# Kernel optimization log

Measured on AMD Instinct MI355X. Metric: run time of the kernel, lower is better.

The kernel has to match this reference:

```python
import jax, jax.numpy as jnp
import numpy as np

LN_EPS = 1e-12  # BERT LayerNorm eps


def _lstm_dir(x, wih, whh, bih, bhh, reverse):
    # x: [T, B, D] -> outputs [T, B, Hd]; torch gate order i, f, g, o
    B = x.shape[1]
    Hd = whh.shape[1]
    b = bih + bhh

    def step(carry, xt):
        h, c = carry
        gates = xt @ wih.T + h @ whh.T + b  # [B, 4*Hd]
        i, f, g, o = jnp.split(gates, 4, axis=-1)
        c = jax.nn.sigmoid(f) * c + jax.nn.sigmoid(i) * jnp.tanh(g)
        h = jax.nn.sigmoid(o) * jnp.tanh(c)
        return (h, c), h

    init = (jnp.zeros((B, Hd), x.dtype), jnp.zeros((B, Hd), x.dtype))
    _, ys = jax.lax.scan(step, init, x, reverse=reverse)
    return ys


def _forward(input_ids, labels, word_emb, pos_emb, type_emb, ln_g, ln_b,
             w_ih, w_hh, b_ih, b_hh, fc_w, fc_b, crf_start, crf_end, crf_trans):
    B, T = input_ids.shape
    # BERT embeddings (eval mode: dropout = identity)
    emb = word_emb[input_ids] + pos_emb[:T][None, :, :] + type_emb[0][None, None, :]
    mu = emb.mean(-1, keepdims=True)
    var = ((emb - mu) ** 2).mean(-1, keepdims=True)
    emb = (emb - mu) / jnp.sqrt(var + LN_EPS) * ln_g + ln_b

    # stacked bidirectional LSTM
    x = emb.transpose(1, 0, 2)  # [T, B, 768]
    n_layers = w_ih.shape[0]
    for l in range(n_layers):
        f = _lstm_dir(x, w_ih[l, 0], w_hh[l, 0], b_ih[l, 0], b_hh[l, 0], False)
        r = _lstm_dir(x, w_ih[l, 1], w_hh[l, 1], b_ih[l, 1], b_hh[l, 1], True)
        x = jnp.concatenate([f, r], axis=-1)  # [T, B, 768]
    out = x.transpose(1, 0, 2)  # [B, T, 768]

    em = out @ fc_w.T + fc_b  # emissions [B, T, C]

    # CRF log-likelihood (full mask, torchcrf reduction='sum')
    gold_em = jnp.take_along_axis(em, labels[..., None], axis=2)[..., 0]  # [B, T]
    score = (crf_start[labels[:, 0]]
             + gold_em.sum(axis=1)
             + crf_trans[labels[:, :-1], labels[:, 1:]].sum(axis=1)
             + crf_end[labels[:, -1]])

    alpha0 = crf_start[None, :] + em[:, 0]  # [B, C]

    def step(alpha, e_t):
        a = jax.nn.logsumexp(alpha[:, :, None] + crf_trans[None, :, :], axis=1) + e_t
        return a, None

    alpha, _ = jax.lax.scan(step, alpha0, em[:, 1:].transpose(1, 0, 2))
    logZ = jax.nn.logsumexp(alpha + crf_end[None, :], axis=1)  # [B]
    return jnp.sum(logZ - score)  # loss = -llh


def setup_inputs() -> dict:
    key = jax.random.key(0)
    ks = jax.random.split(key, 16)
    B, T, V, P, D, C, L, Hd = 32, 256, 30522, 512, 768, 14, 2, 384
    s = 0.05
    return {
        "input_ids": jax.random.randint(ks[0], (B, T), 0, V),
        "labels": jax.random.randint(ks[1], (B, T), 0, C),
        "word_emb": jax.random.normal(ks[2], (V, D), jnp.float32) * 0.02,
        "pos_emb": jax.random.normal(ks[3], (P, D), jnp.float32) * 0.02,
        "type_emb": jax.random.normal(ks[4], (2, D), jnp.float32) * 0.02,
        "ln_g": jnp.ones((D,), jnp.float32),
        "ln_b": jnp.zeros((D,), jnp.float32),
        "w_ih": jax.random.normal(ks[5], (L, 2, 4 * Hd, D), jnp.float32) * s,
        "w_hh": jax.random.normal(ks[6], (L, 2, 4 * Hd, Hd), jnp.float32) * s,
        "b_ih": jax.random.normal(ks[7], (L, 2, 4 * Hd), jnp.float32) * s,
        "b_hh": jax.random.normal(ks[8], (L, 2, 4 * Hd), jnp.float32) * s,
        "fc_w": jax.random.normal(ks[9], (C, D), jnp.float32) * s,
        "fc_b": jnp.zeros((C,), jnp.float32),
        "crf_start": jax.random.normal(ks[10], (C,), jnp.float32) * 0.1,
        "crf_end": jax.random.normal(ks[11], (C,), jnp.float32) * 0.1,
        "crf_trans": jax.random.normal(ks[12], (C, C), jnp.float32) * 0.1,
    }


def reference(input_ids, labels, word_emb, pos_emb, type_emb, ln_g, ln_b,
              w_ih, w_hh, b_ih, b_hh, fc_w, fc_b, crf_start, crf_end, crf_trans):
    return _forward(input_ids, labels, word_emb, pos_emb, type_emb, ln_g, ln_b,
                    w_ih, w_hh, b_ih, b_hh, fc_w, fc_b, crf_start, crf_end, crf_trans)
```

## Files before the change

kernel.cpp:

```cpp
#include <hip/hip_runtime.h>

typedef unsigned short u16;
typedef unsigned long long u64;
typedef __bf16 bfx8 __attribute__((ext_vector_type(8)));
typedef float  fx4  __attribute__((ext_vector_type(4)));

static __device__ __forceinline__ float b2f(u16 u){
  unsigned v = ((unsigned)u) << 16;
  return __builtin_bit_cast(float, v);
}
static __device__ __forceinline__ u16 f2b(float f){
  unsigned u = __builtin_bit_cast(unsigned, f);
  u = (u + 0x7FFFu + ((u >> 16) & 1u)) >> 16;
  return (u16)u;
}
static __device__ __forceinline__ float blo(unsigned v){ return b2f((u16)(v & 0xFFFFu)); }
static __device__ __forceinline__ float bhi(unsigned v){ return b2f((u16)(v >> 16)); }
static __device__ __forceinline__ float sigm(float x){
  float cx = fminf(fmaxf(x, -30.f), 30.f);
  float e = __expf(-cx);
  return __builtin_amdgcn_rcpf(1.f + e);
}
static __device__ __forceinline__ float tanh_f(float x){
  float cx = fminf(fmaxf(x, -15.f), 15.f);
  float e = __expf(2.f * cx);
  return (e - 1.f) * __builtin_amdgcn_rcpf(e + 1.f);
}
static __device__ __forceinline__ u64 ald64(const u64* p){
  return __hip_atomic_load(p, __ATOMIC_RELAXED, __HIP_MEMORY_SCOPE_AGENT);
}
static __device__ __forceinline__ void ast64(u64* p, u64 v){
  __hip_atomic_store(p, v, __ATOMIC_RELAXED, __HIP_MEMORY_SCOPE_AGENT);
}

__global__ __launch_bounds__(256) void embed_ln(
    const int* __restrict__ ids, const float* __restrict__ we,
    const float* __restrict__ pe, const float* __restrict__ te,
    const float* __restrict__ lng, const float* __restrict__ lnb,
    u16* __restrict__ X)
{
  int row = blockIdx.x;
  int t = row >> 5, b = row & 31;
  int id = ids[b * 256 + t];
  int tid = threadIdx.x;
  int wv = tid >> 6, lane = tid & 63;
  __shared__ float red[8];
  float v[3]; float s = 0.f, s2 = 0.f;
  const float* wrow = we + (long)id * 768;
  const float* prow = pe + (long)t * 768;
#pragma unroll
  for (int u = 0; u < 3; ++u){
    int k = tid + 256 * u;
    float x = wrow[k] + prow[k] + te[k];
    v[u] = x; s += x; s2 += x * x;
  }
#pragma unroll
  for (int o = 32; o > 0; o >>= 1){ s += __shfl_xor(s, o); s2 += __shfl_xor(s2, o); }
  if (lane == 0){ red[wv] = s; red[4 + wv] = s2; }
  __syncthreads();
  float S  = red[0] + red[1] + red[2] + red[3];
  float S2 = red[4] + red[5] + red[6] + red[7];
  float mu = S * (1.f / 768.f);
  float var = S2 * (1.f / 768.f) - mu * mu;
  float rs = rsqrtf(var + 1e-12f);
#pragma unroll
  for (int u = 0; u < 3; ++u){
    int k = tid + 256 * u;
    float y = (v[u] - mu) * rs * lng[k] + lnb[k];
    X[(long)row * 768 + k] = f2b(y);
  }
}

__global__ __launch_bounds__(256) void gemm_pre(
    const u16* __restrict__ A,
    const float* __restrict__ W,
    const float* __restrict__ bi,
    const float* __restrict__ bh,
    u16* __restrict__ pre)
{
  __shared__ u16 la[64][40];
  __shared__ u16 lb[64][40];
  int m0 = blockIdx.x * 64, n0 = blockIdx.y * 64;
  int tid = threadIdx.x;
  int wv = tid >> 6, lane = tid & 63;
  int l15 = lane & 15, l4 = lane >> 4;
  int r = tid >> 2, seg = (tid & 3) * 8;
  fx4 acc[4];
#pragma unroll
  for (int i = 0; i < 4; ++i){ acc[i][0]=0.f; acc[i][1]=0.f; acc[i][2]=0.f; acc[i][3]=0.f; }
  for (int k0 = 0; k0 < 768; k0 += 32){
    __syncthreads();
    *reinterpret_cast<uint4*>(&la[r][seg]) =
        *reinterpret_cast<const uint4*>(&A[(long)(m0 + r) * 768 + k0 + seg]);
    {
      const float* src = &W[(long)(n0 + r) * 768 + k0 + seg];
      union { u16 h[8]; uint4 v; } tb;
#pragma unroll
      for (int e = 0; e < 8; ++e) tb.h[e] = f2b(src[e]);
      *reinterpret_cast<uint4*>(&lb[r][seg]) = tb.v;
    }
    __syncthreads();
    bfx8 af = __builtin_bit_cast(bfx8, *reinterpret_cast<const uint4*>(&la[wv * 16 + l15][8 * l4]));
#pragma unroll
    for (int nt = 0; nt < 4; ++nt){
      bfx8 bf = __builtin_bit_cast(bfx8, *reinterpret_cast<const uint4*>(&lb[nt * 16 + l15][8 * l4]));
      acc[nt] = __builtin_amdgcn_mfma_f32_16x16x32_bf16(af, bf, acc[nt], 0, 0, 0);
    }
  }
#pragma unroll
  for (int nt = 0; nt < 4; ++nt){
    int n = n0 + nt * 16 + l15;
    int d = (n >= 1536) ? 1 : 0;
    int np = n - d * 1536;
    float bias = bi[n] + bh[n];
#pragma unroll
    for (int q = 0; q < 4; ++q){
      int m = m0 + wv * 16 + 4 * l4 + q;
      int tt = m >> 5, bb = m & 31;
      float vv = acc[nt][q] + bias;
      pre[((long)((d * 256 + tt) * 32 + bb)) * 1536 + np] = f2b(vv);
    }
  }
}

__global__ __launch_bounds__(256) void lstm_layer(
    const float* __restrict__ Whh,
    const u16*  __restrict__ pre,
    u16* __restrict__ Y,
    u64* __restrict__ H64)
{
  __shared__ u16 lw[64][386];
  __shared__ u16 hb[32][386];
  __shared__ float gl2[4][16][33];
  int wg = blockIdx.x;
  int d = wg / 24, sl = wg - d * 24;
  int js = sl * 16;
  int tid = threadIdx.x;
  int wv = tid >> 6, lane = tid & 63;
  int l15 = lane & 15, l4 = lane >> 4;
  int b0 = tid & 31, q = tid >> 5;
  int jl0 = 2 * q, jl1 = 2 * q + 1;

  ast64(&H64[((long)(1 * 2 + d) * 192 + sl * 8 + q) * 32 + b0], 0ull);

  for (int i = tid; i < 64 * 96; i += 256){
    int rr = i / 96, c4 = i - rr * 96;
    const float* src = Whh + ((long)(d * 1536 + (rr >> 4) * 384 + js + (rr & 15))) * 384 + 4 * c4;
    float4 v = *reinterpret_cast<const float4*>(src);
    short4 pk;
    pk.x = (short)f2b(v.x); pk.y = (short)f2b(v.y);
    pk.z = (short)f2b(v.z); pk.w = (short)f2b(v.w);
    *reinterpret_cast<short4*>(&lw[rr][(4 * c4) ^ (8 * (rr & 7))]) = pk;
  }
  __syncthreads();

  float c0 = 0.f, c1 = 0.f;

  int tfirst = d ? 255 : 0;
  const u16* pb0 = pre + ((long)(d * 256 + tfirst) * 32 + b0) * 1536 + js + jl0;
  uint4 pc;
  pc.x = *reinterpret_cast<const unsigned*>(pb0 + 0 * 384);
  pc.y = *reinterpret_cast<const unsigned*>(pb0 + 1 * 384);
  pc.z = *reinterpret_cast<const unsigned*>(pb0 + 2 * 384);
  pc.w = *reinterpret_cast<const unsigned*>(pb0 + 3 * 384);

  for (int s = 0; s < 256; ++s){
    int tt = d ? (255 - s) : s;
    int pr = (s + 1) & 1;
    int pw = s & 1;

    int sn = (s + 1 < 256) ? (s + 1) : 255;
    int tn = d ? (255 - sn) : sn;
    const u16* pb2 = pre + ((long)(d * 256 + tn) * 32 + b0) * 1536 + js + jl0;
    uint4 pn;
    pn.x = *reinterpret_cast<const unsigned*>(pb2 + 0 * 384);
    pn.y = *reinterpret_cast<const unsigned*>(pb2 + 1 * 384);
    pn.z = *reinterpret_cast<const unsigned*>(pb2 + 2 * 384);
    pn.w = *reinterpret_cast<const unsigned*>(pb2 + 3 * 384);

    {
      const u64* hsrc = H64 + (long)(pr * 2 + d) * 192 * 32;
      unsigned tagv = (unsigned)s;
      for (;;){
        u64 vb[24];
#pragma unroll
        for (int i = 0; i < 24; ++i) vb[i] = ald64(&hsrc[tid + 256 * i]);
        bool ok = true;
#pragma unroll
        for (int i = 0; i < 24; ++i) ok = ok && ((unsigned)(vb[i] >> 32) == tagv);
#pragma unroll
        for (int i = 0; i < 24; ++i){
          int f = tid + 256 * i;
          int bb = f & 31, j2 = f >> 5;
          *reinterpret_cast<unsigned*>(&hb[bb][(2 * j2) ^ (8 * (bb & 7))]) = (unsigned)vb[i];
        }
        if (__syncthreads_and((int)ok)) break;
      }
    }

    fx4 a0a, a0b, a1a, a1b;
#pragma unroll
    for (int z = 0; z < 4; ++z){ a0a[z]=0.f; a0b[z]=0.f; a1a[z]=0.f; a1b[z]=0.f; }
#pragma unroll
    for (int kk = 0; kk < 12; kk += 2){
      int col0 = (kk * 32 + 8 * l4) ^ (8 * (l15 & 7));
      int col1 = ((kk + 1) * 32 + 8 * l4) ^ (8 * (l15 & 7));
      bfx8 bw0 = __builtin_bit_cast(bfx8, *reinterpret_cast<const uint4*>(&lw[wv * 16 + l15][col0]));
      bfx8 h00 = __builtin_bit_cast(bfx8, *reinterpret_cast<const uint4*>(&hb[l15][col0]));
      bfx8 h10 = __builtin_bit_cast(bfx8, *reinterpret_cast<const uint4*>(&hb[16 + l15][col0]));
      bfx8 bw1 = __builtin_bit_cast(bfx8, *reinterpret_cast<const uint4*>(&lw[wv * 16 + l15][col1]));
      bfx8 h01 = __builtin_bit_cast(bfx8, *reinterpret_cast<const uint4*>(&hb[l15][col1]));
      bfx8 h11 = __builtin_bit_cast(bfx8, *reinterpret_cast<const uint4*>(&hb[16 + l15][col1]));
      a0a = __builtin_amdgcn_mfma_f32_16x16x32_bf16(h00, bw0, a0a, 0, 0, 0);
      a1a = __builtin_amdgcn_mfma_f32_16x16x32_bf16(h10, bw0, a1a, 0, 0, 0);
      a0b = __builtin_amdgcn_mfma_f32_16x16x32_bf16(h01, bw1, a0b, 0, 0, 0);
      a1b = __builtin_amdgcn_mfma_f32_16x16x32_bf16(h11, bw1, a1b, 0, 0, 0);
    }
#pragma unroll
    for (int qq = 0; qq < 4; ++qq){
      int bb0 = (4 * l4 + qq) ^ (4 * (l15 & 7));
      int bb1 = (16 + 4 * l4 + qq) ^ (4 * (l15 & 7));
      gl2[wv][l15][bb0] = a0a[qq] + a0b[qq];
      gl2[wv][l15][bb1] = a1a[qq] + a1b[qq];
    }
    __syncthreads();

    int x0 = b0 ^ (4 * (jl0 & 7));
    int x1 = b0 ^ (4 * (jl1 & 7));
    float gi0 = gl2[0][jl0][x0] + blo(pc.x), gi1 = gl2[0][jl1][x1] + bhi(pc.x);
    float gf0 = gl2[1][jl0][x0] + blo(pc.y), gf1 = gl2[1][jl1][x1] + bhi(pc.y);
    float gg0 = gl2[2][jl0][x0] + blo(pc.z), gg1 = gl2[2][jl1][x1] + bhi(pc.z);
    float go0 = gl2[3][jl0][x0] + blo(pc.w), go1 = gl2[3][jl1][x1] + bhi(pc.w);
    c0 = sigm(gf0) * c0 + sigm(gi0) * tanh_f(gg0);
    float h0 = sigm(go0) * tanh_f(c0);
    c1 = sigm(gf1) * c1 + sigm(gi1) * tanh_f(gg1);
    float h1 = sigm(go1) * tanh_f(c1);

    unsigned hv = (unsigned)f2b(h0) | ((unsigned)f2b(h1) << 16);
    ast64(&H64[((long)(pw * 2 + d) * 192 + sl * 8 + q) * 32 + b0],
          ((u64)(unsigned)(s + 1) << 32) | (u64)hv);
    *reinterpret_cast<unsigned*>(&Y[((long)tt * 32 + b0) * 768 + d * 384 + js + jl0]) = hv;
    pc = pn;
  }
}

__global__ __launch_bounds__(256) void fc_em(
    const u16* __restrict__ Y2, const float* __restrict__ fw,
    const float* __restrict__ fb, float* __restrict__ em)
{
  int row = blockIdx.x * 4 + (threadIdx.x >> 6);
  int lane = threadIdx.x & 63;
  float acc[14];
#pragma unroll
  for (int c = 0; c < 14; ++c) acc[c] = 0.f;
#pragma unroll
  for (int u = 0; u < 12; ++u){
    int k = lane + 64 * u;
    float y = b2f(Y2[(long)row * 768 + k]);
#pragma unroll
    for (int c = 0; c < 14; ++c) acc[c] += y * fw[c * 768 + k];
  }
#pragma unroll
  for (int c = 0; c < 14; ++c){
    float a = acc[c];
#pragma unroll
    for (int o = 32; o > 0; o >>= 1) a += __shfl_xor(a, o);
    acc[c] = a;
  }
  if (lane == 0){
    int tt = row >> 5, b = row & 31;
#pragma unroll
    for (int c = 0; c < 14; ++c) em[(long)(b * 256 + tt) * 14 + c] = acc[c] + fb[c];
  }
}

__global__ __launch_bounds__(64) void crf_fwd(
    const float* __restrict__ em,
    const int* __restrict__ labels,
    const float* __restrict__ cs, const float* __restrict__ ce,
    const float* __restrict__ ct,
    float* __restrict__ lossb)
{
  int b = blockIdx.x;
  int lane = threadIdx.x;
  const float* E = em + (long)b * 256 * 14;
  const int* L = labels + b * 256;

  float sc = 0.f;
  for (int t = lane; t < 256; t += 64){
    int lt = L[t];
    sc += E[t * 14 + lt];
    if (t < 255) sc += ct[lt * 14 + L[t + 1]];
  }
#pragma unroll
  for (int o = 32; o > 0; o >>= 1) sc += __shfl_xor(sc, o);
  float score = sc + cs[L[0]] + ce[L[255]];

  __shared__ float al[2][16];
  int j = lane >> 2, ih = lane & 3;
  if (lane < 16){
    al[0][lane] = (lane < 14) ? (cs[lane] + E[lane]) : -1e30f;
    al[1][lane] = -1e30f;
  }
  __syncthreads();
  float tr[4];
#pragma unroll
  for (int w = 0; w < 4; ++w){
    int i = ih * 4 + w;
    tr[w] = (i < 14 && j < 14) ? ct[i * 14 + j] : -1e30f;
  }
  for (int t = 1; t < 256; ++t){
    int par = t & 1;
    float vals[4]; float m = -1e30f;
#pragma unroll
    for (int w = 0; w < 4; ++w){
      int i = ih * 4 + w;
      float v = al[par ^ 1][i] + tr[w];
      vals[w] = v; m = fmaxf(m, v);
    }
    m = fmaxf(m, __shfl_xor(m, 1));
    m = fmaxf(m, __shfl_xor(m, 2));
    float s = 0.f;
#pragma unroll
    for (int w = 0; w < 4; ++w) s += __expf(vals[w] - m);
    s += __shfl_xor(s, 1);
    s += __shfl_xor(s, 2);
    if (ih == 0 && j < 14) al[par][j] = m + __logf(s) + E[t * 14 + j];
    __syncthreads();
  }
  float v = (lane < 14) ? (al[1][lane] + ce[lane]) : -1e30f;
  float mm = v;
#pragma unroll
  for (int o = 32; o > 0; o >>= 1) mm = fmaxf(mm, __shfl_xor(mm, o));
  float ss = (lane < 14) ? __expf(v - mm) : 0.f;
#pragma unroll
  for (int o = 32; o > 0; o >>= 1) ss += __shfl_xor(ss, o);
  if (lane == 0) lossb[b] = (mm + __logf(ss)) - score;
}

__global__ __launch_bounds__(64) void final_sum(const float* __restrict__ lb, float* __restrict__ out){
  int lane = threadIdx.x;
  float v = (lane < 32) ? lb[lane] : 0.f;
#pragma unroll
  for (int o = 32; o > 0; o >>= 1) v += __shfl_xor(v, o);
  if (lane == 0) out[0] = v;
}

extern "C" void kernel_launch(void* const* d_in, const int* in_sizes, int n_in,
                              void* d_out, int out_size, void* d_ws, size_t ws_size,
                              hipStream_t stream)
{
  const int*   ids = (const int*)d_in[0];
  const int*   lab = (const int*)d_in[1];
  const float* we  = (const float*)d_in[2];
  const float* pe  = (const float*)d_in[3];
  const float* te  = (const float*)d_in[4];
  const float* lng = (const float*)d_in[5];
  const float* lnb = (const float*)d_in[6];
  const float* wih = (const float*)d_in[7];
  const float* whh = (const float*)d_in[8];
  const float* bih = (const float*)d_in[9];
  const float* bhh = (const float*)d_in[10];
  const float* fcw = (const float*)d_in[11];
  const float* fcb = (const float*)d_in[12];
  const float* cs  = (const float*)d_in[13];
  const float* ce  = (const float*)d_in[14];
  const float* ct  = (const float*)d_in[15];
  float* out = (float*)d_out;

  char* ws = (char*)d_ws;
  size_t off = 0;
  u16* X0  = (u16*)(ws + off); off += (size_t)8192 * 768 * 2;
  u16* Y1  = (u16*)(ws + off); off += (size_t)8192 * 768 * 2;
  u16* PRE = (u16*)(ws + off); off += (size_t)2 * 256 * 32 * 1536 * 2;
  float* EM = (float*)(ws + off); off += (size_t)32 * 256 * 14 * 4;
  u64* H64a = (u64*)(ws + off); off += (size_t)2 * 2 * 192 * 32 * 8;
  u64* H64b = (u64*)(ws + off); off += (size_t)2 * 2 * 192 * 32 * 8;
  float* LB = (float*)(ws + off); off += 128;
  u16* Y2 = X0;

  embed_ln<<<8192, 256, 0, stream>>>(ids, we, pe, te, lng, lnb, X0);

  gemm_pre<<<dim3(128, 48), 256, 0, stream>>>(X0, wih, bih, bhh, PRE);
  lstm_layer<<<48, 256, 0, stream>>>(whh, PRE, Y1, H64a);
  gemm_pre<<<dim3(128, 48), 256, 0, stream>>>(Y1, wih + (size_t)2 * 1536 * 768,
                                              bih + 2 * 1536, bhh + 2 * 1536, PRE);
  lstm_layer<<<48, 256, 0, stream>>>(whh + (size_t)2 * 1536 * 384, PRE, Y2, H64b);

  fc_em<<<2048, 256, 0, stream>>>(Y2, fcw, fcb, EM);
  crf_fwd<<<32, 64, 0, stream>>>(EM, lab, cs, ce, ct, LB);
  final_sum<<<1, 64, 0, stream>>>(LB, out);
}
```

Measured before the change: 2.417 ms.

## Skip own-slice tag check, prefetch gates two steps ahead, add spin backoff

```diff
diff --git a/kernel.cpp b/kernel.cpp
--- a/kernel.cpp
+++ b/kernel.cpp
@@ -142,6 +142,7 @@
   int jl0 = 2 * q, jl1 = 2 * q + 1;
 
   ast64(&H64[((long)(1 * 2 + d) * 192 + sl * 8 + q) * 32 + b0], 0ull);
+  u64 own_word = 0ull;
 
   for (int i = tid; i < 64 * 96; i += 256){
     int rr = i / 96, c4 = i - rr * 96;
@@ -156,47 +157,59 @@
 
   float c0 = 0.f, c1 = 0.f;
 
-  int tfirst = d ? 255 : 0;
-  const u16* pb0 = pre + ((long)(d * 256 + tfirst) * 32 + b0) * 1536 + js + jl0;
-  uint4 pc;
+  int t0 = d ? 255 : 0;
+  int t1 = d ? 254 : 1;
+  const u16* pb0 = pre + ((long)(d * 256 + t0) * 32 + b0) * 1536 + js + jl0;
+  const u16* pb1 = pre + ((long)(d * 256 + t1) * 32 + b0) * 1536 + js + jl0;
+  uint4 pc, pn;
   pc.x = *reinterpret_cast<const unsigned*>(pb0 + 0 * 384);
   pc.y = *reinterpret_cast<const unsigned*>(pb0 + 1 * 384);
   pc.z = *reinterpret_cast<const unsigned*>(pb0 + 2 * 384);
   pc.w = *reinterpret_cast<const unsigned*>(pb0 + 3 * 384);
+  pn.x = *reinterpret_cast<const unsigned*>(pb1 + 0 * 384);
+  pn.y = *reinterpret_cast<const unsigned*>(pb1 + 1 * 384);
+  pn.z = *reinterpret_cast<const unsigned*>(pb1 + 2 * 384);
+  pn.w = *reinterpret_cast<const unsigned*>(pb1 + 3 * 384);
 
   for (int s = 0; s < 256; ++s){
     int tt = d ? (255 - s) : s;
     int pr = (s + 1) & 1;
     int pw = s & 1;
 
-    int sn = (s + 1 < 256) ? (s + 1) : 255;
-    int tn = d ? (255 - sn) : sn;
-    const u16* pb2 = pre + ((long)(d * 256 + tn) * 32 + b0) * 1536 + js + jl0;
-    uint4 pn;
-    pn.x = *reinterpret_cast<const unsigned*>(pb2 + 0 * 384);
-    pn.y = *reinterpret_cast<const unsigned*>(pb2 + 1 * 384);
-    pn.z = *reinterpret_cast<const unsigned*>(pb2 + 2 * 384);
-    pn.w = *reinterpret_cast<const unsigned*>(pb2 + 3 * 384);
-
     {
       const u64* hsrc = H64 + (long)(pr * 2 + d) * 192 * 32;
       unsigned tagv = (unsigned)s;
+      __builtin_amdgcn_s_sleep(2);
       for (;;){
         u64 vb[24];
 #pragma unroll
         for (int i = 0; i < 24; ++i) vb[i] = ald64(&hsrc[tid + 256 * i]);
         bool ok = true;
 #pragma unroll
-        for (int i = 0; i < 24; ++i) ok = ok && ((unsigned)(vb[i] >> 32) == tagv);
-#pragma unroll
-        for (int i = 0; i < 24; ++i){
-          int f = tid + 256 * i;
-          int bb = f & 31, j2 = f >> 5;
-          *reinterpret_cast<unsigned*>(&hb[bb][(2 * j2) ^ (8 * (bb & 7))]) = (unsigned)vb[i];
+        for (int i = 0; i < 24; ++i)
+          if (i != sl) ok = ok && ((unsigned)(vb[i] >> 32) == tagv);
+        if (__syncthreads_and((int)ok)){
+          vb[sl] = own_word;
+#pragma unroll
+          for (int i = 0; i < 24; ++i){
+            int f = tid + 256 * i;
+            int bb = f & 31, j2 = f >> 5;
+            *reinterpret_cast<unsigned*>(&hb[bb][(2 * j2) ^ (8 * (bb & 7))]) = (unsigned)vb[i];
+          }
+          __syncthreads();
+          break;
         }
-        if (__syncthreads_and((int)ok)) break;
       }
     }
+
+    int s2 = (s + 2 < 256) ? (s + 2) : 255;
+    int t2 = d ? (255 - s2) : s2;
+    const u16* pb2 = pre + ((long)(d * 256 + t2) * 32 + b0) * 1536 + js + jl0;
+    uint4 p2;
+    p2.x = *reinterpret_cast<const unsigned*>(pb2 + 0 * 384);
+    p2.y = *reinterpret_cast<const unsigned*>(pb2 + 1 * 384);
+    p2.z = *reinterpret_cast<const unsigned*>(pb2 + 2 * 384);
+    p2.w = *reinterpret_cast<const unsigned*>(pb2 + 3 * 384);
 
     fx4 a0a, a0b, a1a, a1b;
 #pragma unroll
@@ -237,10 +250,10 @@
     float h1 = sigm(go1) * tanh_f(c1);
 
     unsigned hv = (unsigned)f2b(h0) | ((unsigned)f2b(h1) << 16);
-    ast64(&H64[((long)(pw * 2 + d) * 192 + sl * 8 + q) * 32 + b0],
-          ((u64)(unsigned)(s + 1) << 32) | (u64)hv);
+    own_word = ((u64)(unsigned)(s + 1) << 32) | (u64)hv;
+    ast64(&H64[((long)(pw * 2 + d) * 192 + sl * 8 + q) * 32 + b0], own_word);
     *reinterpret_cast<unsigned*>(&Y[((long)tt * 32 + b0) * 768 + d * 384 + js + jl0]) = hv;
-    pc = pn;
+    pc = pn; pn = p2;
   }
 }
 
```

After: 5.662 ms. 134% more time.
